# Performance work log

Measured on AMD Instinct MI355X. Metric: run time of the kernel, lower is better.

The kernel has to match this reference:

```python
import jax, jax.numpy as jnp
import numpy as np

D_MODEL = 96
D_STATE = 16
D_INNER = 192   # expand * d_model
DT_RANK = 6     # ceil(96/16)
D_DEPTH_OUT = 1024  # (64/2)*(64/2)
BATCH, HH, WW = 2, 64, 64


def silu(v):
    return v * jax.nn.sigmoid(v)


def setup_inputs() -> dict:
    key = jax.random.key(0)
    ks = jax.random.split(key, 10)
    f = jnp.float32
    x = jax.random.normal(ks[0], (BATCH, HH, WW, D_MODEL), f)
    in_proj_w = jax.random.normal(ks[1], (2 * D_INNER, D_MODEL), f) * 0.02
    conv2d_w = jax.random.normal(ks[2], (D_INNER, 1, 3, 3), f) * 0.1  # depthwise, groups=D_INNER
    conv2d_b = jnp.zeros((D_INNER,), f)
    depth_conv_w = jax.random.normal(ks[3], (D_INNER, 1, 3, 3), f) * 0.1  # depthwise, stride 2
    depth_conv_b = jnp.zeros((D_INNER,), f)
    depth_fc_w = jax.random.normal(ks[4], (D_INNER, D_DEPTH_OUT), f) * 0.02
    depth_fc_b = jnp.zeros((D_INNER,), f)
    x_proj_w = jax.random.normal(ks[5], (DT_RANK + 2 * D_STATE, D_INNER), f) * 0.02
    dt_init_std = DT_RANK ** (-0.5)
    dt_projs_w = jax.random.uniform(ks[6], (D_INNER, DT_RANK), f, -dt_init_std, dt_init_std)
    # inverse-softplus of dt ~ U(log 1e-3, log 0.1)
    dt = jnp.exp(jax.random.uniform(ks[7], (D_INNER,), f) * (np.log(0.1) - np.log(0.001)) + np.log(0.001))
    dt = jnp.clip(dt, 1e-4, None)
    dt_projs_b = dt + jnp.log(-jnp.expm1(-dt))
    A_logs = jnp.log(jnp.tile(jnp.arange(1, D_STATE + 1, dtype=f)[None, :], (D_INNER, 1)))
    Ds = jnp.ones((D_INNER,), f)
    out_norm_w = jnp.ones((D_INNER,), f)
    out_norm_b = jnp.zeros((D_INNER,), f)
    out_proj_w = jax.random.normal(ks[8], (D_MODEL, D_INNER), f) * 0.02
    return dict(x=x, in_proj_w=in_proj_w, conv2d_w=conv2d_w, conv2d_b=conv2d_b,
                depth_conv_w=depth_conv_w, depth_conv_b=depth_conv_b,
                depth_fc_w=depth_fc_w, depth_fc_b=depth_fc_b, x_proj_w=x_proj_w,
                dt_projs_w=dt_projs_w, dt_projs_b=dt_projs_b, A_logs=A_logs, Ds=Ds,
                out_norm_w=out_norm_w, out_norm_b=out_norm_b, out_proj_w=out_proj_w)


def _selective_scan(u, delta, A, Bm, Cm, D, delta_bias):
    # u, delta: [B, D, L]; A: [D, N]; Bm, Cm: [B, N, L]; D: [D]; delta_bias: [D]
    delta = jax.nn.softplus(delta + delta_bias[None, :, None])
    dA = jnp.exp(jnp.einsum('bdl,dn->lbdn', delta, A))          # [L,B,D,N]
    dBu = jnp.einsum('bdl,bnl,bdl->lbdn', delta, Bm, u)          # [L,B,D,N]
    Ct = jnp.transpose(Cm, (2, 0, 1))                            # [L,B,N]
    h0 = jnp.zeros(dA.shape[1:], u.dtype)

    def step(h, inp):
        a, b, c = inp
        h = a * h + b                                            # S6 recurrence
        return h, jnp.einsum('bdn,bn->bd', h, c)

    _, ys = jax.lax.scan(step, h0, (dA, dBu, Ct))                # ys: [L,B,D]
    y = jnp.transpose(ys, (1, 2, 0))                             # [B,D,L]
    return y + D[None, :, None] * u


def _forward(x, in_proj_w, conv2d_w, conv2d_b, depth_conv_w, depth_conv_b,
             depth_fc_w, depth_fc_b, x_proj_w, dt_projs_w, dt_projs_b,
             A_logs, Ds, out_norm_w, out_norm_b, out_proj_w):
    B, H, W, _ = x.shape
    Di, N, R = D_INNER, D_STATE, DT_RANK
    dn = ('NCHW', 'OIHW', 'NCHW')
    xz = x @ in_proj_w.T
    x1, z = jnp.split(xz, 2, axis=-1)
    xc = jnp.transpose(x1, (0, 3, 1, 2))                         # [B,Di,H,W]
    xc = jax.lax.conv_general_dilated(xc, conv2d_w, (1, 1), [(1, 1), (1, 1)],
                                      dimension_numbers=dn, feature_group_count=Di)
    xc = silu(xc + conv2d_b[None, :, None, None])
    dxc = jax.lax.conv_general_dilated(xc, depth_conv_w, (2, 2), [(1, 1), (1, 1)],
                                       dimension_numbers=dn, feature_group_count=Di)
    dxc = dxc + depth_conv_b[None, :, None, None]                # [B,Di,H/2,W/2]
    dx = dxc.reshape(B, Di, -1)                                  # [B,Di,1024]
    dx = dx @ depth_fc_w.T + depth_fc_b                          # [B,Di,Di]
    dx = silu(jnp.transpose(dx, (0, 2, 1)))                      # [B,Di,CC], CC=Di
    L = H * W
    CC = dx.shape[-1]
    xs = jnp.concatenate([dx, xc.reshape(B, Di, L)], axis=-1)    # mode='head': [B,Di,LL]
    x_dbl = jnp.einsum('bdl,cd->bcl', xs, x_proj_w)
    dts, Bm, Cm = x_dbl[:, :R], x_dbl[:, R:R + N], x_dbl[:, R + N:]
    dts = jnp.einsum('brl,dr->bdl', dts, dt_projs_w)
    A = -jnp.exp(A_logs)
    y = _selective_scan(xs, dts, A, Bm, Cm, Ds, dt_projs_b)
    y = y[..., CC:]                                              # drop depth tokens (head mode)
    y = jnp.transpose(y, (0, 2, 1)).reshape(B, H, W, Di)
    mu = jnp.mean(y, axis=-1, keepdims=True)
    var = jnp.var(y, axis=-1, keepdims=True)
    y = (y - mu) * jax.lax.rsqrt(var + 1e-5) * out_norm_w + out_norm_b
    y = y * silu(z)
    return y @ out_proj_w.T


def reference(x, in_proj_w, conv2d_w, conv2d_b, depth_conv_w, depth_conv_b,
              depth_fc_w, depth_fc_b, x_proj_w, dt_projs_w, dt_projs_b,
              A_logs, Ds, out_norm_w, out_norm_b, out_proj_w):
    return _forward(x, in_proj_w, conv2d_w, conv2d_b, depth_conv_w, depth_conv_b,
                    depth_fc_w, depth_fc_b, x_proj_w, dt_projs_w, dt_projs_b,
                    A_logs, Ds, out_norm_w, out_norm_b, out_proj_w)
```

## Files before the change

### kernel.cpp

```cpp
#include <hip/hip_runtime.h>
#include <hip/hip_bf16.h>

typedef __hip_bfloat16 bf16;

#define BATCH 2
#define DM 96
#define DI 192
#define LSP 4096
#define LD 192
#define LTOT 4288
#define NST 16
#define RK 6
#define DFC 1024
#define CLEN 64
#define NCH 67
#define SCH 64
#define XR 16
#define NG  (BATCH * DI * NST)

__device__ __forceinline__ float b2f(bf16 v) { return __bfloat162float(v); }
__device__ __forceinline__ float silu_f(float x) { return x / (1.f + __expf(-x)); }
__device__ __forceinline__ float softplus_f(float x) { return x > 20.f ? x : log1pf(__expf(x)); }

__device__ __forceinline__ int is_f32(const void* alog) {
    return ((const unsigned int*)alog)[0] == 0u;
}
__device__ __forceinline__ float LDI(const void* p, int i, int f32m) {
    return f32m ? ((const float*)p)[i] : __bfloat162float(((const bf16*)p)[i]);
}
__device__ __forceinline__ void unpack2(unsigned int u, float* o) {
    o[0] = __uint_as_float(u << 16);
    o[1] = __uint_as_float(u & 0xffff0000u);
}

__global__ __launch_bounds__(768) void k_inproj(const void* __restrict__ x, const void* __restrict__ ipw,
                                                const void* __restrict__ alog,
                                                float* __restrict__ x1, float* __restrict__ z) {
    __shared__ uint4 sxr[384];
    const int f32m = is_f32(alog);
    int t = threadIdx.x;
    int col = t >> 1;
    int kh = t & 1;
    int row0 = blockIdx.x * 16;
    float wr[48];
    if (f32m) {
        const float4* wp = (const float4*)((const float*)ipw + col * 96 + kh * 48);
        #pragma unroll
        for (int i = 0; i < 12; i++) {
            float4 v = wp[i];
            wr[4*i] = v.x; wr[4*i+1] = v.y; wr[4*i+2] = v.z; wr[4*i+3] = v.w;
        }
        if (t < 384) sxr[t] = ((const uint4*)((const float*)x + row0 * 96))[t];
        __syncthreads();
        for (int r = 0; r < 16; r++) {
            const uint4* xr = &sxr[r * 24 + kh * 12];
            float acc = 0.f;
            #pragma unroll
            for (int i = 0; i < 12; i++) {
                uint4 u = xr[i];
                acc += __uint_as_float(u.x) * wr[4*i]   + __uint_as_float(u.y) * wr[4*i+1]
                     + __uint_as_float(u.z) * wr[4*i+2] + __uint_as_float(u.w) * wr[4*i+3];
            }
            acc += __shfl_xor(acc, 1);
            if (kh == 0) {
                int row = row0 + r;
                if (col < DI) x1[row * DI + col] = acc;
                else          z[row * DI + (col - DI)] = acc;
            }
        }
    } else {
        const uint4* wp = (const uint4*)((const bf16*)ipw + col * 96 + kh * 48);
        #pragma unroll
        for (int i = 0; i < 6; i++) {
            uint4 v = wp[i];
            unpack2(v.x, &wr[8*i]);   unpack2(v.y, &wr[8*i+2]);
            unpack2(v.z, &wr[8*i+4]); unpack2(v.w, &wr[8*i+6]);
        }
        if (t < 192) sxr[t] = ((const uint4*)((const bf16*)x + row0 * 96))[t];
        __syncthreads();
        for (int r = 0; r < 16; r++) {
            const uint4* xr = &sxr[r * 12 + kh * 6];
            float acc = 0.f;
            #pragma unroll
            for (int i = 0; i < 6; i++) {
                uint4 xv = xr[i];
                float xf8[8];
                unpack2(xv.x, &xf8[0]); unpack2(xv.y, &xf8[2]);
                unpack2(xv.z, &xf8[4]); unpack2(xv.w, &xf8[6]);
                #pragma unroll
                for (int j = 0; j < 8; j++) acc += xf8[j] * wr[8*i + j];
            }
            acc += __shfl_xor(acc, 1);
            if (kh == 0) {
                int row = row0 + r;
                if (col < DI) x1[row * DI + col] = acc;
                else          z[row * DI + (col - DI)] = acc;
            }
        }
    }
}

__global__ __launch_bounds__(192) void k_conv1(const float* __restrict__ x1, const void* __restrict__ cw,
                                               const void* __restrict__ cb, float* __restrict__ xs,
                                               const void* __restrict__ alog) {
    const int f32m = is_f32(alog);
    int d = threadIdx.x;
    int blk = blockIdx.x;
    int b = blk >> 9;
    int rest = blk & 511;
    int h = rest >> 3, w0 = (rest & 7) * 8;
    float wgt[9];
    #pragma unroll
    for (int i = 0; i < 9; i++) wgt[i] = LDI(cw, d * 9 + i, f32m);
    float bias = LDI(cb, d, f32m);
    float val[3][10];
    #pragma unroll
    for (int dh = 0; dh < 3; dh++) {
        int hh = h + dh - 1;
        #pragma unroll
        for (int j = 0; j < 10; j++) {
            int ww = w0 + j - 1;
            val[dh][j] = ((unsigned)hh < 64u && (unsigned)ww < 64u)
                       ? x1[((b << 12) + (hh << 6) + ww) * DI + d] : 0.f;
        }
    }
    #pragma unroll
    for (int i = 0; i < 8; i++) {
        float acc = bias;
        #pragma unroll
        for (int dh = 0; dh < 3; dh++)
            #pragma unroll
            for (int dw = 0; dw < 3; dw++)
                acc += val[dh][i + dw] * wgt[dh * 3 + dw];
        xs[(b * LTOT + LD + (h << 6) + w0 + i) * DI + d] = silu_f(acc);
    }
}

__global__ __launch_bounds__(192) void k_conv2(const float* __restrict__ xs, const void* __restrict__ dw,
                                               const void* __restrict__ db, float* __restrict__ dxc,
                                               const void* __restrict__ alog) {
    const int f32m = is_f32(alog);
    int d = threadIdx.x;
    int blk = blockIdx.x;
    int b = blk >> 10, lp = blk & 1023;
    int hp = lp >> 5, wp = lp & 31;
    float acc = LDI(db, d, f32m);
    #pragma unroll
    for (int dh = 0; dh < 3; dh++) {
        int h = 2 * hp + dh - 1;
        if ((unsigned)h >= 64u) continue;
        #pragma unroll
        for (int dw_ = 0; dw_ < 3; dw_++) {
            int w_ = 2 * wp + dw_ - 1;
            if ((unsigned)w_ >= 64u) continue;
            acc += xs[(b * LTOT + LD + (h << 6) + w_) * DI + d] * LDI(dw, d * 9 + dh * 3 + dw_, f32m);
        }
    }
    dxc[(b * DFC + lp) * DI + d] = acc;
}

__global__ __launch_bounds__(192) void k_dfc(const float* __restrict__ dxc, const void* __restrict__ fw,
                                             float* __restrict__ part, const void* __restrict__ alog) {
    __shared__ float sfw[4 * 128];
    const int f32m = is_f32(alog);
    int t = threadIdx.x;
    int blk = blockIdx.x;
    int p = blk / 96;
    int rem = blk - p * 96;
    int b   = rem / 48;
    int ch0 = (rem % 48) * 4;
    int k0  = p * 128;
    for (int idx = t; idx < 4 * 128; idx += 192)
        sfw[idx] = LDI(fw, (ch0 + (idx >> 7)) * DFC + k0 + (idx & 127), f32m);
    __syncthreads();
    float a0 = 0.f, a1 = 0.f, a2 = 0.f, a3 = 0.f;
    #pragma unroll 8
    for (int k = 0; k < 128; k++) {
        float dv = dxc[(b * DFC + k0 + k) * DI + t];
        a0 += dv * sfw[k];
        a1 += dv * sfw[128 + k];
        a2 += dv * sfw[256 + k];
        a3 += dv * sfw[384 + k];
    }
    int ob = ((p * 2 + b) * 192 + t) * DI + ch0;
    *(float4*)&part[ob] = make_float4(a0, a1, a2, a3);
}

__global__ __launch_bounds__(256) void k_xdbl(const float* __restrict__ xs_r, float* __restrict__ xs_w,
                                              const float* __restrict__ part, const void* __restrict__ fb,
                                              const void* __restrict__ xpw,
                                              float* __restrict__ BCb, float* __restrict__ dts,
                                              const void* __restrict__ alog) {
    __shared__ float sw[38 * 196];
    __shared__ float srow[XR][196];
    const int f32m = is_f32(alog);
    int t = threadIdx.x;
    for (int c = t >> 3; c < 38; c += 32) {
        int seg = (t & 7) * 24;
        for (int k = seg; k < seg + 24; k++) sw[c * 196 + k] = LDI(xpw, c * DI + k, f32m);
    }
    int row0 = blockIdx.x * XR;
    int bb = row0 >= LTOT ? 1 : 0;
    int depth = (row0 - bb * LTOT) < LD;
    for (int idx = t; idx < XR * DI; idx += 256) {
        int row = idx / DI, k = idx - row * DI;
        int grow = row0 + row;
        float v;
        if (depth) {
            int tok = grow - bb * LTOT;
            int o = (bb * 192 + tok) * DI + k;
            v = 0.f;
            #pragma unroll
            for (int p = 0; p < 8; p++) v += part[o + p * 73728];
            v = silu_f(v + LDI(fb, k, f32m));
            xs_w[grow * DI + k] = v;
        } else {
            v = xs_r[grow * DI + k];
        }
        srow[row][k] = v;
    }
    __syncthreads();
    int r = t & 15, cg = t >> 4;
    float a0 = 0.f, a1 = 0.f, a2 = 0.f;
    const float4* w0 = (const float4*)&sw[cg * 196];
    const float4* w1 = (const float4*)&sw[(cg + 16) * 196];
    const float4* w2 = (const float4*)&sw[(cg < 6 ? cg + 32 : cg) * 196];
    const float4* xr = (const float4*)&srow[r][0];
    #pragma unroll 4
    for (int k = 0; k < 48; k++) {
        float4 xv = xr[k], v0 = w0[k], v1 = w1[k], v2 = w2[k];
        a0 += xv.x * v0.x + xv.y * v0.y + xv.z * v0.z + xv.w * v0.w;
        a1 += xv.x * v1.x + xv.y * v1.y + xv.z * v1.z + xv.w * v1.w;
        a2 += xv.x * v2.x + xv.y * v2.y + xv.z * v2.z + xv.w * v2.w;
    }
    int grow = row0 + r;
    if (cg < 6) dts[grow * 6 + cg] = a0;
    else        BCb[grow * 32 + (cg - 6)] = a0;
    BCb[grow * 32 + (cg + 10)] = a1;
    if (cg < 6) BCb[grow * 32 + (cg + 26)] = a2;
}

__device__ __forceinline__ void delta_block(const float* sdts, const float* sdwb, float* sdel, int t) {
    int e = t * 4;
    int i = e >> 4, dl = e & 15;
    #pragma unroll
    for (int q = 0; q < 4; q++) {
        int dlq = dl + q;
        float dv = sdwb[96 + dlq];
        #pragma unroll
        for (int r2 = 0; r2 < RK; r2++) dv += sdts[i * RK + r2] * sdwb[dlq * RK + r2];
        sdel[e + q] = softplus_f(dv);
    }
}

__global__ __launch_bounds__(256) void k_scan1(const float* __restrict__ dts, const float* __restrict__ xs,
                                               const float* __restrict__ BCb, const void* __restrict__ dtw,
                                               const void* __restrict__ dtb, const void* __restrict__ alog,
                                               float2* __restrict__ AH) {
    __shared__ float su[CLEN * 16];
    __shared__ float sB[CLEN * 16];
    __shared__ float sdel[CLEN * 16];
    __shared__ float sdts[CLEN * RK];
    __shared__ float sdwb[112];
    const int f32m = is_f32(alog);
    int t = threadIdx.x;
    int beta = blockIdx.x;
    int b = beta / (12 * NCH);
    int rem = beta - b * (12 * NCH);
    int dblk = rem / NCH, ch = rem - dblk * NCH;
    int d0 = dblk * 16, l0 = ch * CLEN;
    int bL = b * LTOT;
    {
        int e = t * 4;
        int i = e >> 4, dd = e & 15;
        *(float4*)&su[e] = *(const float4*)&xs[(bL + l0 + i) * DI + d0 + dd];
        *(float4*)&sB[e] = *(const float4*)&BCb[(bL + l0 + i) * 32 + dd];
    }
    for (int idx = t; idx < CLEN * RK; idx += 256) sdts[idx] = dts[(bL + l0) * RK + idx];
    if (t < 96)            sdwb[t] = LDI(dtw, (d0 + t / 6) * RK + (t % 6), f32m);
    else if (t < 112)      sdwb[t] = LDI(dtb, d0 + (t - 96), f32m);
    __syncthreads();
    delta_block(sdts, sdwb, sdel, t);
    __syncthreads();
    int dloc = t >> 4, n = t & 15;
    int d = d0 + dloc;
    float A = -__expf(LDI(alog, d * NST + n, f32m));
    float h = 0.f, ap = 1.f;
    #pragma unroll 4
    for (int i = 0; i < CLEN; i++) {
        float dt = sdel[(i << 4) | dloc];
        float u  = su[(i << 4) | dloc];
        float Bv = sB[(i << 4) | n];
        float a = __expf(dt * A);
        h = a * h + dt * Bv * u;
        ap *= a;
    }
    int g = ((b * DI + d) * NST) + n;
    AH[ch * NG + g] = make_float2(ap, h);
}

__global__ __launch_bounds__(64) void k_scan2(const float2* __restrict__ AH, float* __restrict__ He) {
    int g = blockIdx.x * 64 + threadIdx.x;
    float h = 0.f;
    for (int ch = 0; ch < NCH; ch++) {
        He[ch * NG + g] = h;
        float2 v = AH[ch * NG + g];
        h = v.x * h + v.y;
    }
}

__global__ __launch_bounds__(256) void k_scan3(const float* __restrict__ dts, const float* __restrict__ xs,
                                               const float* __restrict__ BCb, const void* __restrict__ dtw,
                                               const void* __restrict__ dtb, const void* __restrict__ alog,
                                               const void* __restrict__ Dsv, const float* __restrict__ He,
                                               float* __restrict__ y) {
    __shared__ float su[CLEN * 16];
    __shared__ float sbc[CLEN * 32];
    __shared__ float sdel[CLEN * 16];
    __shared__ float sdts[CLEN * RK];
    __shared__ float sdwb[112];
    const int f32m = is_f32(alog);
    int t = threadIdx.x;
    int beta = blockIdx.x;
    int b = beta / (12 * SCH);
    int rem = beta - b * (12 * SCH);
    int dblk = rem / SCH, ch = (rem - dblk * SCH) + 3;
    int d0 = dblk * 16, l0 = ch * CLEN;
    int bL = b * LTOT;
    {
        int e = t * 4;
        int i = e >> 4, dd = e & 15;
        *(float4*)&su[e] = *(const float4*)&xs[(bL + l0 + i) * DI + d0 + dd];
    }
    #pragma unroll
    for (int q = 0; q < 2; q++) {
        int e = (t + q * 256) * 4;
        int i = e >> 5, c = e & 31;
        *(float4*)&sbc[e] = *(const float4*)&BCb[(bL + l0 + i) * 32 + c];
    }
    for (int idx = t; idx < CLEN * RK; idx += 256) sdts[idx] = dts[(bL + l0) * RK + idx];
    if (t < 96)            sdwb[t] = LDI(dtw, (d0 + t / 6) * RK + (t % 6), f32m);
    else if (t < 112)      sdwb[t] = LDI(dtb, d0 + (t - 96), f32m);
    __syncthreads();
    delta_block(sdts, sdwb, sdel, t);
    __syncthreads();
    int dloc = t >> 4, n = t & 15;
    int d = d0 + dloc;
    float A = -__expf(LDI(alog, d * NST + n, f32m));
    float Dv = LDI(Dsv, d, f32m);
    int g = ((b * DI + d) * NST) + n;
    float h = He[ch * NG + g];
    for (int i = 0; i < CLEN; i++) {
        float dt = sdel[(i << 4) | dloc];
        float u  = su[(i << 4) | dloc];
        float Bv = sbc[(i << 5) | n];
        float Cv = sbc[(i << 5) | 16 | n];
        float a = __expf(dt * A);
        h = a * h + dt * Bv * u;
        float yv = h * Cv;
        #pragma unroll
        for (int m = 8; m; m >>= 1) yv += __shfl_xor(yv, m, 16);
        int l = l0 + i;
        if (n == 0) y[(b * LSP + (l - LD)) * DI + d] = yv + Dv * u;
    }
}

__global__ __launch_bounds__(384) void k_out(const float* __restrict__ y, const float* __restrict__ z,
                                             const void* __restrict__ nw, const void* __restrict__ nb,
                                             const void* __restrict__ opw, void* __restrict__ out,
                                             const void* __restrict__ alog) {
    __shared__ float sg[2][DI];
    __shared__ float sred[2][2][3];
    const int f32m = is_f32(alog);
    int t = threadIdx.x;
    int m = t >> 2, kh = t & 3;
    float wr[48];
    if (f32m) {
        const float4* wp = (const float4*)((const float*)opw + m * DI + kh * 48);
        #pragma unroll
        for (int i = 0; i < 12; i++) {
            float4 v = wp[i];
            wr[4*i] = v.x; wr[4*i+1] = v.y; wr[4*i+2] = v.z; wr[4*i+3] = v.w;
        }
    } else {
        const uint4* wp = (const uint4*)((const bf16*)opw + m * DI + kh * 48);
        #pragma unroll
        for (int i = 0; i < 6; i++) {
            uint4 v = wp[i];
            unpack2(v.x, &wr[8*i]);   unpack2(v.y, &wr[8*i+2]);
            unpack2(v.z, &wr[8*i+4]); unpack2(v.w, &wr[8*i+6]);
        }
    }
    float nwv = 0.f, nbv = 0.f;
    if (t < DI) { nwv = LDI(nw, t, f32m); nbv = LDI(nb, t, f32m); }
    int wv_ = t >> 6;
    int row0 = blockIdx.x * 16;
    for (int pr = 0; pr < 8; pr++) {
        int r0 = row0 + pr * 2, r1 = r0 + 1;
        float y0 = 0.f, z0 = 0.f, y1 = 0.f, z1 = 0.f;
        if (t < DI) {
            y0 = y[r0 * DI + t]; z0 = z[r0 * DI + t];
            y1 = y[r1 * DI + t]; z1 = z[r1 * DI + t];
            float s0 = y0, q0 = y0 * y0, s1 = y1, q1 = y1 * y1;
            #pragma unroll
            for (int off = 32; off; off >>= 1) {
                s0 += __shfl_xor(s0, off); q0 += __shfl_xor(q0, off);
                s1 += __shfl_xor(s1, off); q1 += __shfl_xor(q1, off);
            }
            if ((t & 63) == 0) {
                sred[0][0][wv_] = s0; sred[0][1][wv_] = q0;
                sred[1][0][wv_] = s1; sred[1][1][wv_] = q1;
            }
        }
        __syncthreads();
        if (t < DI) {
            float S0  = sred[0][0][0] + sred[0][0][1] + sred[0][0][2];
            float Q0  = sred[0][1][0] + sred[0][1][1] + sred[0][1][2];
            float S1  = sred[1][0][0] + sred[1][0][1] + sred[1][0][2];
            float Q1  = sred[1][1][0] + sred[1][1][1] + sred[1][1][2];
            float mu0 = S0 * (1.f / 192.f), var0 = Q0 * (1.f / 192.f) - mu0 * mu0;
            float mu1 = S1 * (1.f / 192.f), var1 = Q1 * (1.f / 192.f) - mu1 * mu1;
            float g0 = (y0 - mu0) * rsqrtf(var0 + 1e-5f) * nwv + nbv;
            g0 *= z0 / (1.f + __expf(-z0));
            float g1 = (y1 - mu1) * rsqrtf(var1 + 1e-5f) * nwv + nbv;
            g1 *= z1 / (1.f + __expf(-z1));
            sg[0][t] = g0;
            sg[1][t] = g1;
        }
        __syncthreads();
        const float* g0p = &sg[0][kh * 48];
        const float* g1p = &sg[1][kh * 48];
        float a0 = 0.f, a1 = 0.f;
        #pragma unroll
        for (int j = 0; j < 48; j++) {
            a0 += g0p[j] * wr[j];
            a1 += g1p[j] * wr[j];
        }
        a0 += __shfl_xor(a0, 1); a0 += __shfl_xor(a0, 2);
        a1 += __shfl_xor(a1, 1); a1 += __shfl_xor(a1, 2);
        if (kh == 0) {
            if (f32m) {
                ((float*)out)[r0 * DM + m] = a0;
                ((float*)out)[r1 * DM + m] = a1;
            } else {
                ((bf16*)out)[r0 * DM + m] = __float2bfloat16(a0);
                ((bf16*)out)[r1 * DM + m] = __float2bfloat16(a1);
            }
        }
    }
}

extern "C" void kernel_launch(void* const* d_in, const int* in_sizes, int n_in,
                              void* d_out, int out_size, void* d_ws, size_t ws_size,
                              hipStream_t stream) {
    (void)in_sizes; (void)n_in; (void)out_size; (void)ws_size;
    const void* x    = d_in[0];
    const void* ipw  = d_in[1];
    const void* c1w  = d_in[2];
    const void* c1b  = d_in[3];
    const void* c2w  = d_in[4];
    const void* c2b  = d_in[5];
    const void* fcw  = d_in[6];
    const void* fcb  = d_in[7];
    const void* xpw  = d_in[8];
    const void* dtw  = d_in[9];
    const void* dtb  = d_in[10];
    const void* alog = d_in[11];
    const void* Dsv  = d_in[12];
    const void* nw   = d_in[13];
    const void* nb   = d_in[14];
    const void* opw  = d_in[15];

    float* ws  = (float*)d_ws;
    float* x1  = ws;
    float* z   = x1  + BATCH * LSP * DI;
    float* xs  = z   + BATCH * LSP * DI;
    float* dxc = xs  + BATCH * LTOT * DI;
    float* BCb = dxc + BATCH * DFC * DI;
    float* dts = BCb + BATCH * LTOT * 32;
    float2* AH = (float2*)(dts + BATCH * LTOT * RK);
    float* He  = (float*)(AH + NCH * NG);
    float* part = x1;
    float* y    = x1;

    k_inproj<<<dim3(512), dim3(768), 0, stream>>>(x, ipw, alog, x1, z);
    k_conv1 <<<dim3(1024), dim3(DI), 0, stream>>>(x1, c1w, c1b, xs, alog);
    k_conv2 <<<dim3(BATCH * DFC), dim3(DI), 0, stream>>>(xs, c2w, c2b, dxc, alog);
    k_dfc   <<<dim3(768), dim3(DI), 0, stream>>>(dxc, fcw, part, alog);
    k_xdbl  <<<dim3(536), dim3(256), 0, stream>>>(xs, xs, part, fcb, xpw, BCb, dts, alog);
    k_scan1 <<<dim3(BATCH * 12 * NCH), dim3(256), 0, stream>>>(dts, xs, BCb, dtw, dtb, alog, AH);
    k_scan2 <<<dim3(96), dim3(64), 0, stream>>>(AH, He);
    k_scan3 <<<dim3(BATCH * 12 * SCH), dim3(256), 0, stream>>>(dts, xs, BCb, dtw, dtb, alog, Dsv, He, y);
    k_out   <<<dim3(512), dim3(384), 0, stream>>>(y, z, nw, nb, opw, d_out, alog);
}
```

Before: 224.2 us.

## Restructure chunked scan to one thread per channel with all states in registers

Result: slower. 266.4 us (+18.8%).

```diff
diff --git a/kernel.cpp b/kernel.cpp
--- a/kernel.cpp
+++ b/kernel.cpp
@@ -12,9 +12,9 @@
 #define NST 16
 #define RK 6
 #define DFC 1024
-#define CLEN 64
-#define NCH 67
-#define SCH 64
+#define CLEN 32
+#define NCH 134
+#define SCH 128
 #define XR 16
 #define NG  (BATCH * DI * NST)
 
@@ -240,63 +240,62 @@
     if (cg < 6) BCb[grow * 32 + (cg + 26)] = a2;
 }
 
-__device__ __forceinline__ void delta_block(const float* sdts, const float* sdwb, float* sdel, int t) {
-    int e = t * 4;
-    int i = e >> 4, dl = e & 15;
-    #pragma unroll
-    for (int q = 0; q < 4; q++) {
-        int dlq = dl + q;
-        float dv = sdwb[96 + dlq];
-        #pragma unroll
-        for (int r2 = 0; r2 < RK; r2++) dv += sdts[i * RK + r2] * sdwb[dlq * RK + r2];
-        sdel[e + q] = softplus_f(dv);
-    }
-}
-
-__global__ __launch_bounds__(256) void k_scan1(const float* __restrict__ dts, const float* __restrict__ xs,
+__global__ __launch_bounds__(192) void k_scan1(const float* __restrict__ dts, const float* __restrict__ xs,
                                                const float* __restrict__ BCb, const void* __restrict__ dtw,
                                                const void* __restrict__ dtb, const void* __restrict__ alog,
                                                float2* __restrict__ AH) {
-    __shared__ float su[CLEN * 16];
+    __shared__ float sdts[CLEN * RK];
     __shared__ float sB[CLEN * 16];
-    __shared__ float sdel[CLEN * 16];
-    __shared__ float sdts[CLEN * RK];
-    __shared__ float sdwb[112];
     const int f32m = is_f32(alog);
     int t = threadIdx.x;
     int beta = blockIdx.x;
-    int b = beta / (12 * NCH);
-    int rem = beta - b * (12 * NCH);
-    int dblk = rem / NCH, ch = rem - dblk * NCH;
-    int d0 = dblk * 16, l0 = ch * CLEN;
+    int b = beta / NCH, ch = beta - b * NCH;
+    int l0 = ch * CLEN;
     int bL = b * LTOT;
-    {
-        int e = t * 4;
-        int i = e >> 4, dd = e & 15;
-        *(float4*)&su[e] = *(const float4*)&xs[(bL + l0 + i) * DI + d0 + dd];
-        *(float4*)&sB[e] = *(const float4*)&BCb[(bL + l0 + i) * 32 + dd];
-    }
-    for (int idx = t; idx < CLEN * RK; idx += 256) sdts[idx] = dts[(bL + l0) * RK + idx];
-    if (t < 96)            sdwb[t] = LDI(dtw, (d0 + t / 6) * RK + (t % 6), f32m);
-    else if (t < 112)      sdwb[t] = LDI(dtb, d0 + (t - 96), f32m);
+    sdts[t] = dts[(bL + l0) * RK + t];
+    if (t < 128) {
+        int e = t * 4, i = e >> 4, n = e & 15;
+        *(float4*)&sB[e] = *(const float4*)&BCb[(bL + l0 + i) * 32 + n];
+    }
+    int d = t;
+    float A[16], h[16], ap[16];
+    #pragma unroll
+    for (int n = 0; n < 16; n++) {
+        A[n] = -__expf(LDI(alog, d * NST + n, f32m));
+        h[n] = 0.f;
+        ap[n] = 1.f;
+    }
+    float wdt[RK];
+    #pragma unroll
+    for (int r = 0; r < RK; r++) wdt[r] = LDI(dtw, d * RK + r, f32m);
+    float bdt = LDI(dtb, d, f32m);
+    const float* up = xs + (bL + l0) * DI + d;
     __syncthreads();
-    delta_block(sdts, sdwb, sdel, t);
-    __syncthreads();
-    int dloc = t >> 4, n = t & 15;
-    int d = d0 + dloc;
-    float A = -__expf(LDI(alog, d * NST + n, f32m));
-    float h = 0.f, ap = 1.f;
-    #pragma unroll 4
+    #pragma unroll 8
     for (int i = 0; i < CLEN; i++) {
-        float dt = sdel[(i << 4) | dloc];
-        float u  = su[(i << 4) | dloc];
-        float Bv = sB[(i << 4) | n];
-        float a = __expf(dt * A);
-        h = a * h + dt * Bv * u;
-        ap *= a;
-    }
-    int g = ((b * DI + d) * NST) + n;
-    AH[ch * NG + g] = make_float2(ap, h);
+        float dtv = bdt;
+        #pragma unroll
+        for (int r = 0; r < RK; r++) dtv += sdts[i * RK + r] * wdt[r];
+        float dt = softplus_f(dtv);
+        float u = up[i * DI];
+        float du = dt * u;
+        float Bv[16];
+        const float4* Bp = (const float4*)&sB[i << 4];
+        *(float4*)&Bv[0]  = Bp[0];
+        *(float4*)&Bv[4]  = Bp[1];
+        *(float4*)&Bv[8]  = Bp[2];
+        *(float4*)&Bv[12] = Bp[3];
+        #pragma unroll
+        for (int n = 0; n < 16; n++) {
+            float a = __expf(dt * A[n]);
+            h[n] = a * h[n] + du * Bv[n];
+            ap[n] *= a;
+        }
+    }
+    float4* dst = (float4*)&AH[ch * NG + (b * DI + d) * NST];
+    #pragma unroll
+    for (int j = 0; j < 8; j++)
+        dst[j] = make_float4(ap[2*j], h[2*j], ap[2*j+1], h[2*j+1]);
 }
 
 __global__ __launch_bounds__(64) void k_scan2(const float2* __restrict__ AH, float* __restrict__ He) {
@@ -309,59 +308,70 @@
     }
 }
 
-__global__ __launch_bounds__(256) void k_scan3(const float* __restrict__ dts, const float* __restrict__ xs,
+__global__ __launch_bounds__(192) void k_scan3(const float* __restrict__ dts, const float* __restrict__ xs,
                                                const float* __restrict__ BCb, const void* __restrict__ dtw,
                                                const void* __restrict__ dtb, const void* __restrict__ alog,
                                                const void* __restrict__ Dsv, const float* __restrict__ He,
                                                float* __restrict__ y) {
-    __shared__ float su[CLEN * 16];
+    __shared__ float sdts[CLEN * RK];
     __shared__ float sbc[CLEN * 32];
-    __shared__ float sdel[CLEN * 16];
-    __shared__ float sdts[CLEN * RK];
-    __shared__ float sdwb[112];
     const int f32m = is_f32(alog);
     int t = threadIdx.x;
     int beta = blockIdx.x;
-    int b = beta / (12 * SCH);
-    int rem = beta - b * (12 * SCH);
-    int dblk = rem / SCH, ch = (rem - dblk * SCH) + 3;
-    int d0 = dblk * 16, l0 = ch * CLEN;
+    int b = beta / SCH, chx = beta - b * SCH;
+    int ch = chx + 6;
+    int l0 = ch * CLEN;
     int bL = b * LTOT;
-    {
-        int e = t * 4;
-        int i = e >> 4, dd = e & 15;
-        *(float4*)&su[e] = *(const float4*)&xs[(bL + l0 + i) * DI + d0 + dd];
-    }
-    #pragma unroll
-    for (int q = 0; q < 2; q++) {
-        int e = (t + q * 256) * 4;
+    sdts[t] = dts[(bL + l0) * RK + t];
+    for (int e = t * 4; e < CLEN * 32; e += 192 * 4) {
         int i = e >> 5, c = e & 31;
         *(float4*)&sbc[e] = *(const float4*)&BCb[(bL + l0 + i) * 32 + c];
     }
-    for (int idx = t; idx < CLEN * RK; idx += 256) sdts[idx] = dts[(bL + l0) * RK + idx];
-    if (t < 96)            sdwb[t] = LDI(dtw, (d0 + t / 6) * RK + (t % 6), f32m);
-    else if (t < 112)      sdwb[t] = LDI(dtb, d0 + (t - 96), f32m);
+    int d = t;
+    float A[16], h[16];
+    #pragma unroll
+    for (int n = 0; n < 16; n++) A[n] = -__expf(LDI(alog, d * NST + n, f32m));
+    {
+        const float4* hp = (const float4*)&He[ch * NG + (b * DI + d) * NST];
+        *(float4*)&h[0]  = hp[0];
+        *(float4*)&h[4]  = hp[1];
+        *(float4*)&h[8]  = hp[2];
+        *(float4*)&h[12] = hp[3];
+    }
+    float Dv = LDI(Dsv, d, f32m);
+    float wdt[RK];
+    #pragma unroll
+    for (int r = 0; r < RK; r++) wdt[r] = LDI(dtw, d * RK + r, f32m);
+    float bdt = LDI(dtb, d, f32m);
+    const float* up = xs + (bL + l0) * DI + d;
+    float* yp = y + (b * LSP + l0 - LD) * DI + d;
     __syncthreads();
-    delta_block(sdts, sdwb, sdel, t);
-    __syncthreads();
-    int dloc = t >> 4, n = t & 15;
-    int d = d0 + dloc;
-    float A = -__expf(LDI(alog, d * NST + n, f32m));
-    float Dv = LDI(Dsv, d, f32m);
-    int g = ((b * DI + d) * NST) + n;
-    float h = He[ch * NG + g];
+    #pragma unroll 8
     for (int i = 0; i < CLEN; i++) {
-        float dt = sdel[(i << 4) | dloc];
-        float u  = su[(i << 4) | dloc];
-        float Bv = sbc[(i << 5) | n];
-        float Cv = sbc[(i << 5) | 16 | n];
-        float a = __expf(dt * A);
-        h = a * h + dt * Bv * u;
-        float yv = h * Cv;
-        #pragma unroll
-        for (int m = 8; m; m >>= 1) yv += __shfl_xor(yv, m, 16);
-        int l = l0 + i;
-        if (n == 0) y[(b * LSP + (l - LD)) * DI + d] = yv + Dv * u;
+        float dtv = bdt;
+        #pragma unroll
+        for (int r = 0; r < RK; r++) dtv += sdts[i * RK + r] * wdt[r];
+        float dt = softplus_f(dtv);
+        float u = up[i * DI];
+        float du = dt * u;
+        float Bv[16], Cv[16];
+        const float4* Bp = (const float4*)&sbc[i << 5];
+        *(float4*)&Bv[0]  = Bp[0];
+        *(float4*)&Bv[4]  = Bp[1];
+        *(float4*)&Bv[8]  = Bp[2];
+        *(float4*)&Bv[12] = Bp[3];
+        *(float4*)&Cv[0]  = Bp[4];
+        *(float4*)&Cv[4]  = Bp[5];
+        *(float4*)&Cv[8]  = Bp[6];
+        *(float4*)&Cv[12] = Bp[7];
+        float yv = Dv * u;
+        #pragma unroll
+        for (int n = 0; n < 16; n++) {
+            float a = __expf(dt * A[n]);
+            h[n] = a * h[n] + du * Bv[n];
+            yv += h[n] * Cv[n];
+        }
+        yp[i * DI] = yv;
     }
 }
 
@@ -488,8 +498,8 @@
     k_conv2 <<<dim3(BATCH * DFC), dim3(DI), 0, stream>>>(xs, c2w, c2b, dxc, alog);
     k_dfc   <<<dim3(768), dim3(DI), 0, stream>>>(dxc, fcw, part, alog);
     k_xdbl  <<<dim3(536), dim3(256), 0, stream>>>(xs, xs, part, fcb, xpw, BCb, dts, alog);
-    k_scan1 <<<dim3(BATCH * 12 * NCH), dim3(256), 0, stream>>>(dts, xs, BCb, dtw, dtb, alog, AH);
+    k_scan1 <<<dim3(BATCH * NCH), dim3(DI), 0, stream>>>(dts, xs, BCb, dtw, dtb, alog, AH);
     k_scan2 <<<dim3(96), dim3(64), 0, stream>>>(AH, He);
-    k_scan3 <<<dim3(BATCH * 12 * SCH), dim3(256), 0, stream>>>(dts, xs, BCb, dtw, dtb, alog, Dsv, He, y);
+    k_scan3 <<<dim3(BATCH * SCH), dim3(DI), 0, stream>>>(dts, xs, BCb, dtw, dtb, alog, Dsv, He, y);
     k_out   <<<dim3(512), dim3(384), 0, stream>>>(y, z, nw, nb, opw, d_out, alog);
 }
```
